# Kernel optimization log

Measured on AMD Instinct MI355X. Metric: run time of the kernel, lower is better.

## Reference

```python
import jax, jax.numpy as jnp
import numpy as np

MEM_SIZE = 2048
CELL = 64
R_HEADS = 4
IN_SIZE = 512
IFACE = CELL * R_HEADS + CELL + 2 * CELL + 2 * R_HEADS + 5  # 461
DELTA = 1e-6
EPS = 1e-6


def setup_inputs() -> dict:
    key = jax.random.key(0)
    ks = jax.random.split(key, 8)
    b = 256
    return {
        'xi': jax.random.normal(ks[0], (b, IN_SIZE), jnp.float32),
        'W': jax.random.normal(ks[1], (IFACE, IN_SIZE), jnp.float32) * 0.05,
        'gamma': jnp.ones((IFACE,), jnp.float32),
        'beta': jnp.zeros((IFACE,), jnp.float32),
        'memory': jax.random.normal(ks[2], (b, MEM_SIZE, CELL), jnp.float32),
        'read_weights': jax.random.uniform(ks[3], (b, R_HEADS, MEM_SIZE), jnp.float32),
        'write_weights': jax.random.uniform(ks[4], (b, 1, MEM_SIZE), jnp.float32),
        'usage': jax.random.uniform(ks[5], (b, MEM_SIZE), jnp.float32),
    }


def _cosine(mem, keys):
    # mem: (b,m,c), keys: (b,k,c) -> (b,k,m)
    mem_n = mem / (jnp.linalg.norm(mem, axis=-1, keepdims=True) + EPS)
    key_n = keys / (jnp.linalg.norm(keys, axis=-1, keepdims=True) + EPS)
    return jnp.einsum('bkc,bmc->bkm', key_n, mem_n)


def reference(xi, W, gamma, beta, memory, read_weights, write_weights, usage):
    b = xi.shape[0]
    r, k, w, m = R_HEADS, CELL, CELL, MEM_SIZE

    # interface projection + GroupNorm(1, C) over channel dim
    itf = xi @ W.T
    mu = jnp.mean(itf, axis=1, keepdims=True)
    var = jnp.var(itf, axis=1, keepdims=True)
    itf = (itf - mu) / jnp.sqrt(var + 1e-5) * gamma + beta

    c = 0
    read_keys = jnp.tanh(itf[:, c:c + r * k].reshape(b, r, k)); c += r * k
    read_strengths = jax.nn.softplus(itf[:, c:c + r]); c += r
    write_key = jnp.tanh(itf[:, c:c + k].reshape(b, 1, k)); c += k
    write_strength = jax.nn.softplus(itf[:, c]).reshape(b, 1); c += 1
    erase_vec = jax.nn.sigmoid(itf[:, c:c + w].reshape(b, 1, w)); c += w
    write_vec = jnp.tanh(itf[:, c:c + w].reshape(b, 1, w)); c += w
    free_gates = jax.nn.sigmoid(itf[:, c:c + r]); c += r
    alloc_gate = jax.nn.softmax(itf[:, c:c + 3], axis=1); c += 3
    write_gate = jax.nn.sigmoid(itf[:, c]).reshape(b, 1)

    # ---- usage update ----
    u = usage + (1 - usage) * (1 - jnp.prod(1 - write_weights, axis=1))
    psi = jnp.prod(1 - free_gates[:, :, None] * read_weights, axis=1)  # (b,m)
    u = u * psi

    # ---- content weighting for write ----
    wcw = jax.nn.softmax(_cosine(memory, write_key) * write_strength[:, :, None], axis=2)  # (b,1,m)

    # ---- allocation ----
    u2 = DELTA + (1 - DELTA) * u
    idx = jnp.argsort(u2, axis=1)                              # ascending usage (phi)
    su = jnp.take_along_axis(u2, idx, axis=1)                  # sorted usage
    cp = jnp.cumprod(jnp.concatenate([jnp.ones((b, 1), u2.dtype), su], axis=1), axis=1)[:, :-1]
    sa = (1 - su) * cp
    inv = jnp.argsort(idx, axis=1)                             # inverse permutation (phi_rev)
    alloc = jnp.take_along_axis(sa, inv, axis=1)               # (b,m)

    # ---- write weighting ----
    fw = (alloc_gate[:, 0:1] * jnp.mean(read_weights, axis=1)
          + alloc_gate[:, 1:2] * alloc
          + alloc_gate[:, 2:3] * wcw[:, 0])
    ww = (write_gate * fw)[:, None, :]                         # (b,1,m)

    # ---- memory write (erase + add) ----
    reset_gate = jnp.prod(1 - ww[:, :, :, None] * erase_vec[:, :, None, :], axis=1)  # (b,m,w)
    mem = memory * reset_gate + jnp.einsum('bm,bw->bmw', ww[:, 0], write_vec[:, 0])

    # ---- read ----
    rw = jax.nn.softmax(_cosine(mem, read_keys) * read_strengths[:, :, None], axis=2)  # (b,r,m)
    read_vectors = jnp.einsum('brm,bmw->brw', rw, mem)         # (b,r,w)
    return read_vectors
```

## Files before the change

### kernel.cpp

```cpp
#include <hip/hip_runtime.h>
#include <math.h>

#define MM    2048
#define CC    64
#define RH    4
#define NIF   461
#define INS   512
#define EPSN  1e-6f

typedef unsigned long long u64;

#define OFF_P     ((size_t)0)
#define OFF_U2    ((size_t)131072)
#define OFF_MRW   ((size_t)655360)
#define OFF_ALLOC ((size_t)1179648)
#define OFF_SCAL  ((size_t)1703936)
#define OFF_W8    ((size_t)10092544)
#define OFF_CR    ((size_t)14286848)
#define OFF_PART  ((size_t)14287872)

__global__ __launch_bounds__(512) void k1_interface(
    const float* __restrict__ xi, const float* __restrict__ W,
    const float* __restrict__ gamma, const float* __restrict__ beta,
    const float* __restrict__ read_w, const float* __restrict__ write_w,
    const float* __restrict__ usage, float* __restrict__ ws)
{
  const int b = blockIdx.x, tid = threadIdx.x;
  const int lane = tid & 63, wid = tid >> 6;
  __shared__ __align__(16) float s_xi[512], s_itf[512], s_act[512];
  __shared__ float sRed[24];

  s_xi[tid] = xi[(size_t)b*INS + tid];
  __syncthreads();

  {
    const float4 x0 = ((const float4*)s_xi)[lane*2];
    const float4 x1 = ((const float4*)s_xi)[lane*2+1];
    for (int col = wid; col < NIF; col += 8) {
      const float4* Wr = (const float4*)(W + (size_t)col*INS);
      float4 a0 = Wr[lane*2], a1 = Wr[lane*2+1];
      float p = a0.x*x0.x + a0.y*x0.y + a0.z*x0.z + a0.w*x0.w
              + a1.x*x1.x + a1.y*x1.y + a1.z*x1.z + a1.w*x1.w;
      #pragma unroll
      for (int off=1; off<64; off<<=1) p += __shfl_xor(p, off);
      if (lane==0) s_itf[col] = p;
    }
  }
  __syncthreads();

  {
    float v = (tid < NIF) ? s_itf[tid] : 0.f;
    float s = v, q = v*v;
    #pragma unroll
    for (int off=1; off<64; off<<=1) { s += __shfl_xor(s,off); q += __shfl_xor(q,off); }
    if (lane==0){ sRed[wid] = s; sRed[8+wid] = q; }
    __syncthreads();
    if (tid==0){
      float ts=0.f, tq=0.f;
      for (int i=0;i<8;i++){ ts+=sRed[i]; tq+=sRed[8+i]; }
      float mean = ts/(float)NIF;
      float var  = tq/(float)NIF - mean*mean;
      sRed[16]=mean; sRed[17]=rsqrtf(var+1e-5f);
    }
    __syncthreads();
    float mean = sRed[16], rstd = sRed[17];
    if (tid < NIF) {
      float g = (s_itf[tid]-mean)*rstd*gamma[tid] + beta[tid];
      float a;
      if      (tid < 256) a = tanhf(g);
      else if (tid < 260) a = fmaxf(g,0.f) + log1pf(expf(-fabsf(g)));
      else if (tid < 324) a = tanhf(g);
      else if (tid ==324) a = fmaxf(g,0.f) + log1pf(expf(-fabsf(g)));
      else if (tid < 389) a = 1.f/(1.f+expf(-g));
      else if (tid < 453) a = tanhf(g);
      else if (tid < 457) a = 1.f/(1.f+expf(-g));
      else if (tid < 460) a = g;
      else                a = 1.f/(1.f+expf(-g));
      s_act[tid] = a;
    }
  }
  __syncthreads();

  float* P = ws + OFF_P + (size_t)b*512;
  if (wid < 4) {
    float t = s_act[wid*64 + lane];
    float q = t*t;
    #pragma unroll
    for (int off=1; off<64; off<<=1) q += __shfl_xor(q,off);
    P[wid*64+lane] = t * (s_act[256+wid] / (sqrtf(q) + EPSN));
  } else if (wid == 4) {
    float t = s_act[260+lane];
    float q = t*t;
    #pragma unroll
    for (int off=1; off<64; off<<=1) q += __shfl_xor(q,off);
    P[256+lane] = t * (s_act[324] / (sqrtf(q) + EPSN));
  } else if (wid == 5) {
    P[320+lane] = s_act[325+lane];
    P[384+lane] = s_act[389+lane];
  } else if (wid == 6 && lane == 0) {
    float a0=s_act[457], a1=s_act[458], a2=s_act[459];
    float mx = fmaxf(a0, fmaxf(a1,a2));
    float e0=expf(a0-mx), e1=expf(a1-mx), e2=expf(a2-mx);
    float is = 1.f/(e0+e1+e2);
    P[448]=e0*is; P[449]=e1*is; P[450]=e2*is; P[451]=s_act[460];
  }

  {
    const float4* us4 = (const float4*)(usage   + (size_t)b*MM);
    const float4* wr4 = (const float4*)(write_w + (size_t)b*MM);
    const float4* rw4 = (const float4*)(read_w  + (size_t)b*RH*MM);
    const float fg0=s_act[453], fg1=s_act[454], fg2=s_act[455], fg3=s_act[456];
    float4 u = us4[tid], w = wr4[tid];
    float4 r0 = rw4[tid], r1 = rw4[512+tid], r2 = rw4[1024+tid], r3 = rw4[1536+tid];
    float4 mr, u2o;
    mr.x = 0.25f*(r0.x+r1.x+r2.x+r3.x);
    mr.y = 0.25f*(r0.y+r1.y+r2.y+r3.y);
    mr.z = 0.25f*(r0.z+r1.z+r2.z+r3.z);
    mr.w = 0.25f*(r0.w+r1.w+r2.w+r3.w);
    #define U2C(comp)                                                           \
    { float uu  = u.comp + (1.f-u.comp)*w.comp;                                 \
      float psi = (1.f-fg0*r0.comp)*(1.f-fg1*r1.comp)*(1.f-fg2*r2.comp)*(1.f-fg3*r3.comp); \
      u2o.comp = 1e-6f + (1.f-1e-6f)*(uu*psi); }
    U2C(x) U2C(y) U2C(z) U2C(w)
    #undef U2C
    ((float4*)(ws + OFF_MRW + (size_t)b*MM))[tid] = mr;
    ((float4*)(ws + OFF_U2  + (size_t)b*MM))[tid] = u2o;
  }
}

__global__ __launch_bounds__(256) void k2_fused(
    const float* __restrict__ memory, float* __restrict__ ws)
{
  __shared__ __align__(16) u64 sKeys[2048];
  __shared__ float sT[260];
  const int tid = threadIdx.x;

  if (blockIdx.x < 256) {
    const int b = blockIdx.x;
    const int lane = tid & 63, w = tid >> 6;
    const float* u2p = ws + OFF_U2 + (size_t)b*MM;
    for (int i = tid; i < MM; i += 256)
      sKeys[i] = ((u64)__float_as_uint(u2p[i])<<32) | (unsigned)i;
    __syncthreads();

    for (int k = 2; k <= MM; k <<= 1) {
      for (int j = k >> 1; j > 0; j >>= 1) {
        #pragma unroll 4
        for (int c = tid; c < MM/2; c += 256) {
          int i   = ((c & ~(j-1)) << 1) | (c & (j-1));
          int ixj = i | j;
          u64 a = sKeys[i], d = sKeys[ixj];
          bool up = ((i & k) == 0);
          if ((a > d) == up) { sKeys[i] = d; sKeys[ixj] = a; }
        }
        __syncthreads();
      }
    }

    float p[8];
    {
      float run = 1.f;
      #pragma unroll
      for (int e = 0; e < 8; ++e) {
        float su = __uint_as_float((unsigned)(sKeys[tid*8+e]>>32));
        run *= su; p[e] = run;
      }
      sT[tid] = run;
    }
    __syncthreads();
    float v = sT[tid];
    float incl = v;
    #pragma unroll
    for (int off=1; off<64; off<<=1) {
      float n = __shfl_up(incl, off);
      if (lane >= off) incl *= n;
    }
    float excl = __shfl_up(incl, 1);
    if (lane == 0) excl = 1.f;
    if (lane == 63) sT[256 + w] = incl;
    __syncthreads();
    float base = 1.f;
    for (int ww2 = 0; ww2 < w; ++ww2) base *= sT[256 + ww2];
    float E = base * excl;

    float* allocp = ws + OFF_ALLOC + (size_t)b*MM;
    #pragma unroll
    for (int e = 0; e < 8; ++e) {
      u64 kk = sKeys[tid*8+e];
      float su = __uint_as_float((unsigned)(kk>>32));
      unsigned idx = (unsigned)(kk & 0xFFFFFFFFu);
      float cp = E * (e ? p[e-1] : 1.f);
      allocp[idx] = (1.f - su) * cp;
    }
  } else {
    const int f = blockIdx.x - 256;
    const int b = f >> 3, slice = f & 7;
    const int q = tid & 7, rowg = tid >> 3;
    const float* P = ws + OFF_P + (size_t)b*512;
    const float4 wkA = ((const float4*)(P+256))[q*2], wkB = ((const float4*)(P+256))[q*2+1];
    const float4 eA  = ((const float4*)(P+320))[q*2], eB  = ((const float4*)(P+320))[q*2+1];
    const float4 wvA = ((const float4*)(P+384))[q*2], wvB = ((const float4*)(P+384))[q*2+1];
    const float4 k0A = ((const float4*)P)[      q*2], k0B = ((const float4*)P)[      q*2+1];
    const float4 k1A = ((const float4*)P)[ 16 + q*2], k1B = ((const float4*)P)[ 16 + q*2+1];
    const float4 k2A = ((const float4*)P)[ 32 + q*2], k2B = ((const float4*)P)[ 32 + q*2+1];
    const float4 k3A = ((const float4*)P)[ 48 + q*2], k3B = ((const float4*)P)[ 48 + q*2+1];
    const float4* mem4 = (const float4*)(memory + (size_t)b*MM*CC) + (size_t)slice*256*16;
    float4* sc4 = (float4*)(ws + OFF_SCAL) + ((size_t)b*MM + slice*256)*4;

    for (int it = 0; it < 8; ++it) {
      int m = it*32 + rowg;
      float4 vA = mem4[m*16 + q*2], vB = mem4[m*16 + q*2+1];
      float4 veA, veB;
      veA.x=vA.x*eA.x; veA.y=vA.y*eA.y; veA.z=vA.z*eA.z; veA.w=vA.w*eA.w;
      veB.x=vB.x*eB.x; veB.y=vB.y*eB.y; veB.z=vB.z*eB.z; veB.w=vB.w*eB.w;
      #define DOT(a,b) (a.x*b.x + a.y*b.y + a.z*b.z + a.w*b.w)
      float S  = DOT(vA,wkA) + DOT(vB,wkB);
      float A  = DOT(vA,vA)  + DOT(vB,vB);
      float B  = DOT(veA,vA) + DOT(veB,vB);
      float C  = DOT(veA,veA)+ DOT(veB,veB);
      float D  = DOT(vA,wvA) + DOT(vB,wvB);
      float E  = DOT(veA,wvA)+ DOT(veB,wvB);
      float G0 = DOT(vA,k0A) + DOT(vB,k0B);
      float G1 = DOT(vA,k1A) + DOT(vB,k1B);
      float G2 = DOT(vA,k2A) + DOT(vB,k2B);
      float G3 = DOT(vA,k3A) + DOT(vB,k3B);
      float H0 = DOT(veA,k0A)+ DOT(veB,k0B);
      float H1 = DOT(veA,k1A)+ DOT(veB,k1B);
      float H2 = DOT(veA,k2A)+ DOT(veB,k2B);
      float H3 = DOT(veA,k3A)+ DOT(veB,k3B);
      #undef DOT
      #pragma unroll
      for (int off=1; off<8; off<<=1) {
        S += __shfl_xor(S,off);   A += __shfl_xor(A,off);
        B += __shfl_xor(B,off);   C += __shfl_xor(C,off);
        D += __shfl_xor(D,off);   E += __shfl_xor(E,off);
        G0 += __shfl_xor(G0,off); G1 += __shfl_xor(G1,off);
        G2 += __shfl_xor(G2,off); G3 += __shfl_xor(G3,off);
        H0 += __shfl_xor(H0,off); H1 += __shfl_xor(H1,off);
        H2 += __shfl_xor(H2,off); H3 += __shfl_xor(H3,off);
      }
      if (q == 0) {
        float4 o0; o0.x=S;  o0.y=A;  o0.z=B;  o0.w=C;
        float4 o1; o1.x=D;  o1.y=E;  o1.z=0;  o1.w=0;
        float4 o2; o2.x=G0; o2.y=G1; o2.z=G2; o2.w=G3;
        float4 o3; o3.x=H0; o3.y=H1; o3.z=H2; o3.w=H3;
        sc4[m*4+0]=o0; sc4[m*4+1]=o1; sc4[m*4+2]=o2; sc4[m*4+3]=o3;
      }
    }
  }
}

__global__ __launch_bounds__(512) void k3_weights(float* __restrict__ ws)
{
  const int b = blockIdx.x, tid = threadIdx.x;
  const int lane = tid & 63, w = tid >> 6;
  __shared__ float sEw[2048];
  __shared__ float sWw[2048];
  __shared__ float sE0[2048], sE1[2048], sE2[2048], sE3[2048];
  __shared__ float sR[64];
  __shared__ float sKF[8];

  const float* P = ws + OFF_P + (size_t)b*512;
  const float4* sc4 = (const float4*)(ws + OFF_SCAL + (size_t)b*MM*16);

  if (tid < 64) {
    float wv = P[384+tid];
    float p0=wv*P[tid], p1=wv*P[64+tid], p2=wv*P[128+tid], p3=wv*P[192+tid], f=wv*wv;
    #pragma unroll
    for (int off=1; off<64; off<<=1) {
      p0+=__shfl_xor(p0,off); p1+=__shfl_xor(p1,off); p2+=__shfl_xor(p2,off);
      p3+=__shfl_xor(p3,off); f+=__shfl_xor(f,off);
    }
    if (tid==0){ sKF[0]=p0; sKF[1]=p1; sKF[2]=p2; sKF[3]=p3; sKF[4]=f; }
  }

  float ls = 0.f;
  #pragma unroll
  for (int k = 0; k < 4; ++k) {
    int m = tid + k*512;
    float4 s0 = sc4[m*4];
    float ew = expf(s0.x / (sqrtf(s0.y)+EPSN));
    sEw[m] = ew;
    ls += ew;
  }
  #pragma unroll
  for (int off=1; off<64; off<<=1) ls += __shfl_xor(ls,off);
  if (lane==0) sR[w] = ls;
  __syncthreads();
  const float invW = 1.f/(sR[0]+sR[1]+sR[2]+sR[3]+sR[4]+sR[5]+sR[6]+sR[7]);

  const float ag0=P[448], ag1=P[449], ag2=P[450], wg=P[451];
  const float K0=sKF[0], K1=sKF[1], K2=sKF[2], K3=sKF[3], F=sKF[4];
  const float* mrwp = ws + OFF_MRW   + (size_t)b*MM;
  const float* alp  = ws + OFF_ALLOC + (size_t)b*MM;

  float h0=0.f,h1=0.f,h2=0.f,h3=0.f;
  #pragma unroll
  for (int k = 0; k < 4; ++k) {
    int m = tid + k*512;
    float wwv = wg*(ag0*mrwp[m] + ag1*alp[m] + ag2*sEw[m]*invW);
    sWw[m] = wwv;
    float4 s0 = sc4[m*4], s1 = sc4[m*4+1], sG = sc4[m*4+2], sH = sc4[m*4+3];
    float nsq = s0.y + 2.f*wwv*(s1.x - s0.z) + wwv*wwv*(s0.w - 2.f*s1.y + F);
    float rstd = 1.f/(sqrtf(fmaxf(nsq,0.f))+EPSN);
    float e0 = expf((sG.x + wwv*(K0 - sH.x))*rstd);
    float e1 = expf((sG.y + wwv*(K1 - sH.y))*rstd);
    float e2 = expf((sG.z + wwv*(K2 - sH.z))*rstd);
    float e3 = expf((sG.w + wwv*(K3 - sH.w))*rstd);
    sE0[m]=e0; sE1[m]=e1; sE2[m]=e2; sE3[m]=e3;
    h0+=e0; h1+=e1; h2+=e2; h3+=e3;
  }
  #pragma unroll
  for (int off=1; off<64; off<<=1) {
    h0+=__shfl_xor(h0,off); h1+=__shfl_xor(h1,off);
    h2+=__shfl_xor(h2,off); h3+=__shfl_xor(h3,off);
  }
  if (lane==0){ sR[8+w*4]=h0; sR[9+w*4]=h1; sR[10+w*4]=h2; sR[11+w*4]=h3; }
  __syncthreads();
  float t0=0.f,t1=0.f,t2=0.f,t3=0.f;
  #pragma unroll
  for (int g=0; g<8; ++g){ t0+=sR[8+g*4]; t1+=sR[9+g*4]; t2+=sR[10+g*4]; t3+=sR[11+g*4]; }
  const float i0=1.f/t0, i1=1.f/t1, i2=1.f/t2, i3=1.f/t3;

  float4* w84 = (float4*)(ws + OFF_W8 + (size_t)b*MM*8);
  float cr0=0.f, cr1=0.f, cr2=0.f, cr3=0.f;
  #pragma unroll
  for (int k = 0; k < 4; ++k) {
    int m = tid + k*512;
    float wwv = sWw[m];
    float a0 = sE0[m]*i0, a1 = sE1[m]*i1, a2 = sE2[m]*i2, a3 = sE3[m]*i3;
    float4 oa; oa.x=a0; oa.y=a1; oa.z=a2; oa.w=a3;
    float4 og; og.x=a0*wwv; og.y=a1*wwv; og.z=a2*wwv; og.w=a3*wwv;
    w84[m*2] = oa; w84[m*2+1] = og;
    cr0 += og.x; cr1 += og.y; cr2 += og.z; cr3 += og.w;
  }
  #pragma unroll
  for (int off=1; off<64; off<<=1) {
    cr0+=__shfl_xor(cr0,off); cr1+=__shfl_xor(cr1,off);
    cr2+=__shfl_xor(cr2,off); cr3+=__shfl_xor(cr3,off);
  }
  if (lane==0){ sR[32+w*4]=cr0; sR[33+w*4]=cr1; sR[34+w*4]=cr2; sR[35+w*4]=cr3; }
  __syncthreads();
  if (tid < 4) {
    float s = 0.f;
    #pragma unroll
    for (int g=0; g<8; ++g) s += sR[32+g*4+tid];
    ws[OFF_CR + (size_t)b*4 + tid] = s;
  }
}

__global__ __launch_bounds__(256) void k4_reduce(
    const float* __restrict__ memory, const float* __restrict__ ws,
    float* __restrict__ wso)
{
  const int slice = blockIdx.x, b = blockIdx.y;
  const int tid = threadIdx.x;
  const int w = tid >> 6, lane = tid & 63;
  const int rq = lane >> 4, cq = lane & 15;
  __shared__ __align__(16) float ldsW8[256*8];
  __shared__ __align__(16) float ldsP[4*16*32];

  {
    const float4* g = (const float4*)(ws + OFF_W8 + ((size_t)b*MM + slice*256)*8);
    ((float4*)ldsW8)[tid] = g[tid];
    ((float4*)ldsW8)[tid+256] = g[tid+256];
  }
  __syncthreads();

  const float4* mem4 = (const float4*)(memory + (size_t)b*MM*CC) + (size_t)slice*256*16;
  float4 acc[8];
  #pragma unroll
  for (int j=0;j<8;++j){ acc[j].x=0;acc[j].y=0;acc[j].z=0;acc[j].w=0; }

  #pragma unroll 4
  for (int i = 0; i < 16; ++i) {
    int m = w*64 + i*4 + rq;
    float4 v = mem4[m*16 + cq];
    float4 wa = *(const float4*)&ldsW8[m*8];
    float4 wb = *(const float4*)&ldsW8[m*8+4];
    #define ACC(j, s) { acc[j].x += (s)*v.x; acc[j].y += (s)*v.y; acc[j].z += (s)*v.z; acc[j].w += (s)*v.w; }
    ACC(0, wa.x) ACC(1, wa.y) ACC(2, wa.z) ACC(3, wa.w)
    ACC(4, wb.x) ACC(5, wb.y) ACC(6, wb.z) ACC(7, wb.w)
    #undef ACC
  }
  #pragma unroll
  for (int j=0;j<8;++j){
    #pragma unroll
    for (int off=16; off<64; off<<=1) {
      acc[j].x += __shfl_xor(acc[j].x, off);
      acc[j].y += __shfl_xor(acc[j].y, off);
      acc[j].z += __shfl_xor(acc[j].z, off);
      acc[j].w += __shfl_xor(acc[j].w, off);
    }
  }
  if (rq == 0) {
    float4* p4 = (float4*)&ldsP[(w*16 + cq)*32];
    #pragma unroll
    for (int j=0;j<8;++j) p4[j] = acc[j];
  }
  __syncthreads();
  {
    int jj = tid >> 6;
    int c  = tid & 63;
    int cq2 = c >> 2, ci = c & 3;
    float s1 = 0.f, s2 = 0.f;
    #pragma unroll
    for (int g=0; g<4; ++g) {
      s1 += ldsP[(g*16 + cq2)*32 +  jj*4    + ci];
      s2 += ldsP[(g*16 + cq2)*32 + (jj+4)*4 + ci];
    }
    float* part = wso + OFF_PART + (((size_t)b*8 + slice)*8)*64;
    part[ jj   *64 + c] = s1;
    part[(jj+4)*64 + c] = s2;
  }
}

__global__ __launch_bounds__(256) void k5_combine(
    const float* __restrict__ ws, float* __restrict__ out)
{
  const int b = blockIdx.x, tid = threadIdx.x;
  const int h = tid >> 6, c = tid & 63;
  const float* P = ws + OFF_P + (size_t)b*512;
  float S1 = 0.f, S2 = 0.f;
  #pragma unroll
  for (int s = 0; s < 8; ++s) {
    const float* part = ws + OFF_PART + (((size_t)b*8 + s)*8)*64;
    S1 += part[ h   *64 + c];
    S2 += part[(h+4)*64 + c];
  }
  float e  = P[320+c];
  float wv = P[384+c];
  float cr = ws[OFF_CR + (size_t)b*4 + h];
  out[((size_t)b<<8) + h*64 + c] = S1 - e*S2 + cr*wv;
}

extern "C" void kernel_launch(void* const* d_in, const int* in_sizes, int n_in,
                              void* d_out, int out_size, void* d_ws, size_t ws_size,
                              hipStream_t stream) {
  const float* xi      = (const float*)d_in[0];
  const float* W       = (const float*)d_in[1];
  const float* gamma   = (const float*)d_in[2];
  const float* beta    = (const float*)d_in[3];
  const float* memory  = (const float*)d_in[4];
  const float* read_w  = (const float*)d_in[5];
  const float* write_w = (const float*)d_in[6];
  const float* usage   = (const float*)d_in[7];
  float* ws  = (float*)d_ws;
  float* out = (float*)d_out;

  k1_interface<<<dim3(256), dim3(512), 0, stream>>>(xi, W, gamma, beta, read_w, write_w, usage, ws);
  k2_fused   <<<dim3(2304), dim3(256), 0, stream>>>(memory, ws);
  k3_weights <<<dim3(256), dim3(512), 0, stream>>>(ws);
  k4_reduce  <<<dim3(8,256), dim3(256), 0, stream>>>(memory, ws, ws);
  k5_combine <<<dim3(256), dim3(256), 0, stream>>>(ws, out);
}
```

Before: 136.9 us.

## Fuse weight computation, memory reduction and combine into one kernel with atomics

Merges k3_weights, k4_reduce and k5_combine into a single kernel launched per (slice, batch). Each block redundantly recomputes the full-row softmax normalizers and keeps only its own slice's weights in LDS, then accumulates output via atomicAdd after a memset. This removes two launches and the global round trips for the W8 weights, CR and partial sums. In exchange every slice block repeats the whole-row exp and sqrt work, multiplying that compute roughly eightfold, and introduces float atomics whose summation order is nondeterministic.

```diff
diff --git a/kernel.cpp b/kernel.cpp
--- a/kernel.cpp
+++ b/kernel.cpp
@@ -15,9 +15,6 @@
 #define OFF_MRW   ((size_t)655360)
 #define OFF_ALLOC ((size_t)1179648)
 #define OFF_SCAL  ((size_t)1703936)
-#define OFF_W8    ((size_t)10092544)
-#define OFF_CR    ((size_t)14286848)
-#define OFF_PART  ((size_t)14287872)
 
 __global__ __launch_bounds__(512) void k1_interface(
     const float* __restrict__ xi, const float* __restrict__ W,
@@ -250,14 +247,16 @@
   }
 }
 
-__global__ __launch_bounds__(512) void k3_weights(float* __restrict__ ws)
+__global__ __launch_bounds__(256) void k3_fused(
+    const float* __restrict__ memory, float* __restrict__ ws,
+    float* __restrict__ out)
 {
-  const int b = blockIdx.x, tid = threadIdx.x;
-  const int lane = tid & 63, w = tid >> 6;
-  __shared__ float sEw[2048];
-  __shared__ float sWw[2048];
-  __shared__ float sE0[2048], sE1[2048], sE2[2048], sE3[2048];
-  __shared__ float sR[64];
+  const int slice = blockIdx.x >> 8, b = blockIdx.x & 255;
+  const int tid = threadIdx.x, lane = tid & 63, w = tid >> 6;
+  __shared__ __align__(16) float bufA[2048];
+  __shared__ float bufB[256*5];
+  __shared__ __align__(16) float ldsP[4*16*32];
+  __shared__ float sR[48];
   __shared__ float sKF[8];
 
   const float* P = ws + OFF_P + (size_t)b*512;
@@ -276,30 +275,29 @@
 
   float ls = 0.f;
   #pragma unroll
-  for (int k = 0; k < 4; ++k) {
-    int m = tid + k*512;
+  for (int k = 0; k < 8; ++k) {
+    int m = tid + k*256;
     float4 s0 = sc4[m*4];
     float ew = expf(s0.x / (sqrtf(s0.y)+EPSN));
-    sEw[m] = ew;
+    bufA[m] = ew;
     ls += ew;
   }
   #pragma unroll
   for (int off=1; off<64; off<<=1) ls += __shfl_xor(ls,off);
   if (lane==0) sR[w] = ls;
   __syncthreads();
-  const float invW = 1.f/(sR[0]+sR[1]+sR[2]+sR[3]+sR[4]+sR[5]+sR[6]+sR[7]);
+  const float invW = 1.f/(sR[0]+sR[1]+sR[2]+sR[3]);
 
   const float ag0=P[448], ag1=P[449], ag2=P[450], wg=P[451];
   const float K0=sKF[0], K1=sKF[1], K2=sKF[2], K3=sKF[3], F=sKF[4];
   const float* mrwp = ws + OFF_MRW   + (size_t)b*MM;
   const float* alp  = ws + OFF_ALLOC + (size_t)b*MM;
 
-  float h0=0.f,h1=0.f,h2=0.f,h3=0.f;
-  #pragma unroll
-  for (int k = 0; k < 4; ++k) {
-    int m = tid + k*512;
-    float wwv = wg*(ag0*mrwp[m] + ag1*alp[m] + ag2*sEw[m]*invW);
-    sWw[m] = wwv;
+  float h0=0.f,h1=0.f,h2=0.f,h3=0.f, g0=0.f,g1=0.f,g2=0.f,g3=0.f;
+  #pragma unroll
+  for (int k = 0; k < 8; ++k) {
+    int m = tid + k*256;
+    float wwv = wg*(ag0*mrwp[m] + ag1*alp[m] + ag2*bufA[m]*invW);
     float4 s0 = sc4[m*4], s1 = sc4[m*4+1], sG = sc4[m*4+2], sH = sc4[m*4+3];
     float nsq = s0.y + 2.f*wwv*(s1.x - s0.z) + wwv*wwv*(s0.w - 2.f*s1.y + F);
     float rstd = 1.f/(sqrtf(fmaxf(nsq,0.f))+EPSN);
@@ -307,77 +305,54 @@
     float e1 = expf((sG.y + wwv*(K1 - sH.y))*rstd);
     float e2 = expf((sG.z + wwv*(K2 - sH.z))*rstd);
     float e3 = expf((sG.w + wwv*(K3 - sH.w))*rstd);
-    sE0[m]=e0; sE1[m]=e1; sE2[m]=e2; sE3[m]=e3;
     h0+=e0; h1+=e1; h2+=e2; h3+=e3;
+    g0+=e0*wwv; g1+=e1*wwv; g2+=e2*wwv; g3+=e3*wwv;
+    if (k == slice) {
+      bufB[tid]=e0; bufB[256+tid]=e1; bufB[512+tid]=e2; bufB[768+tid]=e3;
+      bufB[1024+tid]=wwv;
+    }
   }
   #pragma unroll
   for (int off=1; off<64; off<<=1) {
     h0+=__shfl_xor(h0,off); h1+=__shfl_xor(h1,off);
     h2+=__shfl_xor(h2,off); h3+=__shfl_xor(h3,off);
-  }
-  if (lane==0){ sR[8+w*4]=h0; sR[9+w*4]=h1; sR[10+w*4]=h2; sR[11+w*4]=h3; }
-  __syncthreads();
-  float t0=0.f,t1=0.f,t2=0.f,t3=0.f;
-  #pragma unroll
-  for (int g=0; g<8; ++g){ t0+=sR[8+g*4]; t1+=sR[9+g*4]; t2+=sR[10+g*4]; t3+=sR[11+g*4]; }
-  const float i0=1.f/t0, i1=1.f/t1, i2=1.f/t2, i3=1.f/t3;
-
-  float4* w84 = (float4*)(ws + OFF_W8 + (size_t)b*MM*8);
-  float cr0=0.f, cr1=0.f, cr2=0.f, cr3=0.f;
-  #pragma unroll
-  for (int k = 0; k < 4; ++k) {
-    int m = tid + k*512;
-    float wwv = sWw[m];
-    float a0 = sE0[m]*i0, a1 = sE1[m]*i1, a2 = sE2[m]*i2, a3 = sE3[m]*i3;
-    float4 oa; oa.x=a0; oa.y=a1; oa.z=a2; oa.w=a3;
-    float4 og; og.x=a0*wwv; og.y=a1*wwv; og.z=a2*wwv; og.w=a3*wwv;
-    w84[m*2] = oa; w84[m*2+1] = og;
-    cr0 += og.x; cr1 += og.y; cr2 += og.z; cr3 += og.w;
-  }
-  #pragma unroll
-  for (int off=1; off<64; off<<=1) {
-    cr0+=__shfl_xor(cr0,off); cr1+=__shfl_xor(cr1,off);
-    cr2+=__shfl_xor(cr2,off); cr3+=__shfl_xor(cr3,off);
-  }
-  if (lane==0){ sR[32+w*4]=cr0; sR[33+w*4]=cr1; sR[34+w*4]=cr2; sR[35+w*4]=cr3; }
-  __syncthreads();
-  if (tid < 4) {
-    float s = 0.f;
-    #pragma unroll
-    for (int g=0; g<8; ++g) s += sR[32+g*4+tid];
-    ws[OFF_CR + (size_t)b*4 + tid] = s;
-  }
-}
-
-__global__ __launch_bounds__(256) void k4_reduce(
-    const float* __restrict__ memory, const float* __restrict__ ws,
-    float* __restrict__ wso)
-{
-  const int slice = blockIdx.x, b = blockIdx.y;
-  const int tid = threadIdx.x;
-  const int w = tid >> 6, lane = tid & 63;
+    g0+=__shfl_xor(g0,off); g1+=__shfl_xor(g1,off);
+    g2+=__shfl_xor(g2,off); g3+=__shfl_xor(g3,off);
+  }
+  if (lane==0){
+    sR[8 +w*8+0]=h0; sR[8 +w*8+1]=h1; sR[8 +w*8+2]=h2; sR[8 +w*8+3]=h3;
+    sR[8 +w*8+4]=g0; sR[8 +w*8+5]=g1; sR[8 +w*8+6]=g2; sR[8 +w*8+7]=g3;
+  }
+  __syncthreads();
+  const float i0 = 1.f/(sR[8] +sR[16]+sR[24]+sR[32]);
+  const float i1 = 1.f/(sR[9] +sR[17]+sR[25]+sR[33]);
+  const float i2 = 1.f/(sR[10]+sR[18]+sR[26]+sR[34]);
+  const float i3 = 1.f/(sR[11]+sR[19]+sR[27]+sR[35]);
+  const float cr0 = (sR[12]+sR[20]+sR[28]+sR[36])*i0;
+  const float cr1 = (sR[13]+sR[21]+sR[29]+sR[37])*i1;
+  const float cr2 = (sR[14]+sR[22]+sR[30]+sR[38])*i2;
+  const float cr3 = (sR[15]+sR[23]+sR[31]+sR[39])*i3;
+
+  {
+    float e0=bufB[tid], e1=bufB[256+tid], e2=bufB[512+tid], e3=bufB[768+tid];
+    float wwv=bufB[1024+tid];
+    float a0=e0*i0, a1=e1*i1, a2=e2*i2, a3=e3*i3;
+    bufA[tid*8+0]=a0; bufA[tid*8+1]=a1; bufA[tid*8+2]=a2; bufA[tid*8+3]=a3;
+    bufA[tid*8+4]=a0*wwv; bufA[tid*8+5]=a1*wwv; bufA[tid*8+6]=a2*wwv; bufA[tid*8+7]=a3*wwv;
+  }
+  __syncthreads();
+
   const int rq = lane >> 4, cq = lane & 15;
-  __shared__ __align__(16) float ldsW8[256*8];
-  __shared__ __align__(16) float ldsP[4*16*32];
-
-  {
-    const float4* g = (const float4*)(ws + OFF_W8 + ((size_t)b*MM + slice*256)*8);
-    ((float4*)ldsW8)[tid] = g[tid];
-    ((float4*)ldsW8)[tid+256] = g[tid+256];
-  }
-  __syncthreads();
-
   const float4* mem4 = (const float4*)(memory + (size_t)b*MM*CC) + (size_t)slice*256*16;
   float4 acc[8];
   #pragma unroll
   for (int j=0;j<8;++j){ acc[j].x=0;acc[j].y=0;acc[j].z=0;acc[j].w=0; }
-
   #pragma unroll 4
   for (int i = 0; i < 16; ++i) {
     int m = w*64 + i*4 + rq;
     float4 v = mem4[m*16 + cq];
-    float4 wa = *(const float4*)&ldsW8[m*8];
-    float4 wb = *(const float4*)&ldsW8[m*8+4];
+    float4 wa = *(const float4*)&bufA[m*8];
+    float4 wb = *(const float4*)&bufA[m*8+4];
     #define ACC(j, s) { acc[j].x += (s)*v.x; acc[j].y += (s)*v.y; acc[j].z += (s)*v.z; acc[j].w += (s)*v.w; }
     ACC(0, wa.x) ACC(1, wa.y) ACC(2, wa.z) ACC(3, wa.w)
     ACC(4, wb.x) ACC(5, wb.y) ACC(6, wb.z) ACC(7, wb.w)
@@ -399,6 +374,7 @@
     for (int j=0;j<8;++j) p4[j] = acc[j];
   }
   __syncthreads();
+
   {
     int jj = tid >> 6;
     int c  = tid & 63;
@@ -409,29 +385,10 @@
       s1 += ldsP[(g*16 + cq2)*32 +  jj*4    + ci];
       s2 += ldsP[(g*16 + cq2)*32 + (jj+4)*4 + ci];
     }
-    float* part = wso + OFF_PART + (((size_t)b*8 + slice)*8)*64;
-    part[ jj   *64 + c] = s1;
-    part[(jj+4)*64 + c] = s2;
-  }
-}
-
-__global__ __launch_bounds__(256) void k5_combine(
-    const float* __restrict__ ws, float* __restrict__ out)
-{
-  const int b = blockIdx.x, tid = threadIdx.x;
-  const int h = tid >> 6, c = tid & 63;
-  const float* P = ws + OFF_P + (size_t)b*512;
-  float S1 = 0.f, S2 = 0.f;
-  #pragma unroll
-  for (int s = 0; s < 8; ++s) {
-    const float* part = ws + OFF_PART + (((size_t)b*8 + s)*8)*64;
-    S1 += part[ h   *64 + c];
-    S2 += part[(h+4)*64 + c];
-  }
-  float e  = P[320+c];
-  float wv = P[384+c];
-  float cr = ws[OFF_CR + (size_t)b*4 + h];
-  out[((size_t)b<<8) + h*64 + c] = S1 - e*S2 + cr*wv;
+    float crv = (jj==0)?cr0:((jj==1)?cr1:((jj==2)?cr2:cr3));
+    float val = s1 - P[320+c]*s2 + crv*P[384+c]*0.125f;
+    atomicAdd(&out[((size_t)b<<8) + jj*64 + c], val);
+  }
 }
 
 extern "C" void kernel_launch(void* const* d_in, const int* in_sizes, int n_in,
@@ -448,9 +405,8 @@
   float* ws  = (float*)d_ws;
   float* out = (float*)d_out;
 
+  hipMemsetAsync(out, 0, (size_t)out_size*sizeof(float), stream);
   k1_interface<<<dim3(256), dim3(512), 0, stream>>>(xi, W, gamma, beta, read_w, write_w, usage, ws);
   k2_fused   <<<dim3(2304), dim3(256), 0, stream>>>(memory, ws);
-  k3_weights <<<dim3(256), dim3(512), 0, stream>>>(ws);
-  k4_reduce  <<<dim3(8,256), dim3(256), 0, stream>>>(memory, ws, ws);
-  k5_combine <<<dim3(256), dim3(256), 0, stream>>>(ws, out);
+  k3_fused   <<<dim3(2048), dim3(256), 0, stream>>>(memory, ws, out);
 }
```

Measured after the change: 155.9 us. 1.14x slower.
